# Optimization experiments

Hardware: AMD Instinct MI355X
Metric: run time of the kernel (lower is better)

Reference implementation:

```python
import jax, jax.numpy as jnp
import numpy as np

# dims
N = 2048      # total nodes (64 graphs x 32 nodes)
G = 64        # n_graphs
D = 512       # hidden_dim
H = 8         # n_heads
HD = D // H   # head_dim
E = 16        # edge_features
M = 16384     # n_edges


def setup_inputs() -> dict:
    key = jax.random.key(0)
    ks = jax.random.split(key, 12)
    s = 0.02  # param init scale
    inp = {
        "nodes": jax.random.normal(ks[0], (N, D), jnp.float32),
        "edges": jax.random.normal(ks[1], (M, E), jnp.float32),
        "Wq": jax.random.normal(ks[2], (D, D), jnp.float32) * s,
        "bq": jnp.zeros((D,), jnp.float32),
        "Wk": jax.random.normal(ks[3], (D, D), jnp.float32) * s,
        "bk": jnp.zeros((D,), jnp.float32),
        "Wv": jax.random.normal(ks[4], (D, D), jnp.float32) * s,
        "bv": jnp.zeros((D,), jnp.float32),
        "Wo": jax.random.normal(ks[5], (D, D), jnp.float32) * s,
        "bo": jnp.zeros((D,), jnp.float32),
        "We": jax.random.normal(ks[6], (E, H), jnp.float32) * s,
        "be": jnp.zeros((H,), jnp.float32),
        # 64 graphs of exactly 32 nodes each (sums to N, as jraph requires)
        "n_node": jnp.full((G,), N // G, dtype=jnp.int32),
        "senders": jax.random.randint(ks[7], (M,), 0, N, dtype=jnp.int32),
        "receivers": jax.random.randint(ks[8], (M,), 0, N, dtype=jnp.int32),
    }
    return inp


def reference(nodes, edges, Wq, bq, Wk, bk, Wv, bv, Wo, bo, We, be,
              n_node, senders, receivers):
    scale = HD ** -0.5
    # projections -> [N, H, HD]
    q = (nodes @ Wq + bq).reshape(N, H, HD)
    k = (nodes @ Wk + bk).reshape(N, H, HD)
    v = (nodes @ Wv + bv).reshape(N, H, HD)

    # dense scores [N, N, H]
    attn_scores = jnp.einsum('ihd,jhd->ijh', q, k) * scale

    # block-diagonal graph mask
    graph_indices = jnp.repeat(jnp.arange(G), n_node, total_repeat_length=N)
    same_graph = graph_indices[:, None] == graph_indices[None, :]
    attn_scores = attn_scores + jnp.where(same_graph[:, :, None], 0.0, -1e9)

    # edge bias: project edge features to per-head bias, scatter into [N, N, H]
    edge_bias = edges @ We + be                              # [M, H]
    edge_bias_matrix = jnp.zeros((N, N, H), attn_scores.dtype)
    edge_bias_matrix = edge_bias_matrix.at[receivers, senders].set(edge_bias)
    attn_scores = attn_scores + edge_bias_matrix

    # softmax over keys (axis=1, matching the original)
    attn_weights = jax.nn.softmax(attn_scores, axis=1)

    out = jnp.einsum('ijh,jhd->ihd', attn_weights, v).reshape(N, D)
    return out @ Wo + bo
```

## Files before the change

### kernel.cpp

```cpp
#include <hip/hip_runtime.h>

constexpr int N_NODES = 2048;
constexpr int G       = 64;
constexpr int D       = 512;
constexpr int H       = 8;
constexpr int HD      = 64;
constexpr int E       = 16;
constexpr int M_EDGES = 16384;

typedef __attribute__((ext_vector_type(8))) _Float16 f16x8;
typedef __attribute__((ext_vector_type(4))) float f32x4;

__device__ __forceinline__ void load_lds16(const void* g, void* l) {
    __builtin_amdgcn_global_load_lds(
        (const __attribute__((address_space(1))) unsigned int*)g,
        (__attribute__((address_space(3))) unsigned int*)l, 16, 0, 0);
}

__global__ __launch_bounds__(256) void prep_kernel(
    const float* __restrict__ nodes,
    const float* __restrict__ Wq, const float* __restrict__ Wk,
    const float* __restrict__ Wv, const float* __restrict__ Wo,
    _Float16* __restrict__ nA16, _Float16* __restrict__ wT16)
{
    const int bid = blockIdx.x;
    const int t   = threadIdx.x;

    if (bid < 512) {
        int i = bid * 256 + t;
        float4 v0 = ((const float4*)nodes)[2 * i];
        float4 v1 = ((const float4*)nodes)[2 * i + 1];
        float f[8] = { v0.x, v0.y, v0.z, v0.w, v1.x, v1.y, v1.z, v1.w };
        union { _Float16 h[8]; int4 v; } p;
#pragma unroll
        for (int e = 0; e < 8; ++e) p.h[e] = (_Float16)f[e];
        ((int4*)nA16)[i] = p.v;
        return;
    }

    {
        int idx = bid - 512;
        int z   = idx >> 8;
        int rem = idx & 255;
        int k0  = (rem >> 4) * 32, n0 = (rem & 15) * 32;
        const float* W = (z == 0) ? Wq : (z == 1) ? Wk : (z == 2) ? Wv : Wo;
        __shared__ float tile[32][33];
        {
            int kr = t >> 3, nc4 = (t & 7) * 4;
            float4 v = *(const float4*)(W + (size_t)(k0 + kr) * D + n0 + nc4);
            tile[nc4 + 0][kr] = v.x;
            tile[nc4 + 1][kr] = v.y;
            tile[nc4 + 2][kr] = v.z;
            tile[nc4 + 3][kr] = v.w;
        }
        __syncthreads();
        {
            int nl = t >> 3, kq = (t & 7) * 4;
            union { _Float16 h[4]; uint2 v; } hi;
#pragma unroll
            for (int j = 0; j < 4; ++j)
                hi.h[j] = (_Float16)tile[nl][kq + j];
            size_t base = (size_t)z * D * D + (size_t)(n0 + nl) * D + k0 + kq;
            *(uint2*)(wT16 + base) = hi.v;
        }
    }
}

template <typename CT>
__device__ __forceinline__ void gemm_body(
    const _Float16* __restrict__ A, const _Float16* __restrict__ B,
    const float* __restrict__ bias, CT* __restrict__ C,
    int row0, int col0)
{
    __shared__ __align__(16) char lds[2][2][8192];

    const int t    = threadIdx.x;
    const int lane = t & 63;
    const int w    = t >> 6;
    const int wm   = w >> 1, wn = w & 1;

    const int prow0 = t >> 3;
    const int lslot = (t & 7) ^ (prow0 & 7);

    auto stage = [&](int buf, int k0) {
        size_t a0 = (size_t)(row0 + prow0) * 1024 + k0 * 2 + lslot * 16;
        size_t a1 = a0 + 32 * 1024;
        size_t b0 = (size_t)(col0 + prow0) * 1024 + k0 * 2 + lslot * 16;
        size_t b1 = b0 + 32 * 1024;
        load_lds16((const char*)A + a0, &lds[buf][0][t * 16]);
        load_lds16((const char*)A + a1, &lds[buf][0][4096 + t * 16]);
        load_lds16((const char*)B + b0, &lds[buf][1][t * 16]);
        load_lds16((const char*)B + b1, &lds[buf][1][4096 + t * 16]);
    };

    f32x4 acc[2][2] = {};

    stage(0, 0);
    __syncthreads();

    int cur = 0;
    for (int step = 0; step < 8; ++step) {
        if (step < 7) stage(cur ^ 1, (step + 1) * 64);

        f16x8 fa[2][2], fb[2][2];
#pragma unroll
        for (int mf = 0; mf < 2; ++mf) {
            int row = wm * 32 + mf * 16 + (lane & 15);
#pragma unroll
            for (int ks = 0; ks < 2; ++ks) {
                int ps = ((ks * 4 + (lane >> 4)) ^ (row & 7)) << 4;
                fa[mf][ks] = *(const f16x8*)&lds[cur][0][row * 128 + ps];
            }
        }
#pragma unroll
        for (int nf = 0; nf < 2; ++nf) {
            int row = wn * 32 + nf * 16 + (lane & 15);
#pragma unroll
            for (int ks = 0; ks < 2; ++ks) {
                int ps = ((ks * 4 + (lane >> 4)) ^ (row & 7)) << 4;
                fb[nf][ks] = *(const f16x8*)&lds[cur][1][row * 128 + ps];
            }
        }
#pragma unroll
        for (int mf = 0; mf < 2; ++mf)
#pragma unroll
            for (int nf = 0; nf < 2; ++nf)
#pragma unroll
                for (int ks = 0; ks < 2; ++ks)
                    acc[mf][nf] = __builtin_amdgcn_mfma_f32_16x16x32_f16(
                        fa[mf][ks], fb[nf][ks], acc[mf][nf], 0, 0, 0);

        __syncthreads();
        cur ^= 1;
    }

#pragma unroll
    for (int mf = 0; mf < 2; ++mf)
#pragma unroll
        for (int nf = 0; nf < 2; ++nf) {
            int col = col0 + wn * 32 + nf * 16 + (lane & 15);
            float bv = bias[col];
#pragma unroll
            for (int r = 0; r < 4; ++r) {
                int row = row0 + wm * 32 + mf * 16 + (lane >> 4) * 4 + r;
                C[(size_t)row * D + col] = (CT)(acc[mf][nf][r] + bv);
            }
        }
}

struct GemmArgs {
    const _Float16 *A, *BT;
    const float* bias[3];
    void* C;
};

__global__ __launch_bounds__(256) void gemm_qkv_kernel(GemmArgs a)
{
    const int z = blockIdx.z;
    gemm_body<_Float16>(a.A, a.BT + (size_t)z * D * D, a.bias[z],
                        (_Float16*)a.C + (size_t)z * (size_t)N_NODES * D,
                        blockIdx.y * 64, blockIdx.x * 64);
}

__global__ __launch_bounds__(256) void gemm_out_kernel(GemmArgs a)
{
    gemm_body<float>(a.A, a.BT, a.bias[0], (float*)a.C,
                     blockIdx.y * 64, blockIdx.x * 64);
}

__global__ __launch_bounds__(1024) void attn_kernel(
    const _Float16* __restrict__ QKV16,
    const float* __restrict__ edges, const float* __restrict__ We,
    const float* __restrict__ be,
    const int* __restrict__ snd, const int* __restrict__ rcv,
    _Float16* __restrict__ AO16)
{
    const int g = blockIdx.x;
    const int h = blockIdx.y;
    __shared__ float Qs[32][64];
    __shared__ float Ks[32][65];
    __shared__ float Vs[32][65];
    __shared__ float P[32][33];
    __shared__ int   win[1024];
    __shared__ float WesH[E];

    const int t = threadIdx.x;
    win[t] = -1;
    if (t < E) WesH[t] = We[t * H + h];

    const _Float16* Q16 = QKV16;
    const _Float16* K16 = QKV16 + (size_t)N_NODES * D;
    const _Float16* V16 = QKV16 + (size_t)2 * N_NODES * D;
    for (int idx = t; idx < 32 * 64; idx += 1024) {
        int n = idx >> 6, d = idx & 63;
        size_t ga = (size_t)(g * 32 + n) * D + h * HD + d;
        Qs[n][d] = (float)Q16[ga];
        Ks[n][d] = (float)K16[ga];
        Vs[n][d] = (float)V16[ga];
    }
    __syncthreads();

    for (int it = 0; it < M_EDGES / 1024; ++it) {
        int m = it * 1024 + t;
        int s = snd[m], r = rcv[m];
        if ((s >> 5) == g && (r >> 5) == g)
            atomicMax(&win[((r & 31) << 5) | (s & 31)], m);
    }
    __syncthreads();

    const int i = t >> 5;
    const int j = t & 31;
    float s = 0.f;
#pragma unroll
    for (int d = 0; d < 64; ++d) s += Qs[i][d] * Ks[j][d];
    s *= 0.125f;

    int m = win[(i << 5) | j];
    if (m >= 0) {
        float v = be[h];
#pragma unroll
        for (int e = 0; e < E; ++e) v += edges[m * E + e] * WesH[e];
        s += v;
    }

    float mx = s;
#pragma unroll
    for (int o = 16; o > 0; o >>= 1) mx = fmaxf(mx, __shfl_xor(mx, o));
    float p = __expf(s - mx);
    float sum = p;
#pragma unroll
    for (int o = 16; o > 0; o >>= 1) sum += __shfl_xor(sum, o);
    p /= sum;
    P[i][j] = p;
    __syncthreads();

    float o0 = 0.f, o1 = 0.f;
#pragma unroll
    for (int kk = 0; kk < 32; ++kk) {
        float pv = P[i][kk];
        o0 += pv * Vs[kk][j];
        o1 += pv * Vs[kk][j + 32];
    }
    size_t oa = (size_t)(g * 32 + i) * D + h * HD;
    AO16[oa + j]      = (_Float16)o0;
    AO16[oa + j + 32] = (_Float16)o1;
}

extern "C" void kernel_launch(void* const* d_in, const int* in_sizes, int n_in,
                              void* d_out, int out_size, void* d_ws, size_t ws_size,
                              hipStream_t stream)
{
    const float* nodes = (const float*)d_in[0];
    const float* edges = (const float*)d_in[1];
    const float* Wq    = (const float*)d_in[2];
    const float* bq    = (const float*)d_in[3];
    const float* Wk    = (const float*)d_in[4];
    const float* bk    = (const float*)d_in[5];
    const float* Wv    = (const float*)d_in[6];
    const float* bv    = (const float*)d_in[7];
    const float* Wo    = (const float*)d_in[8];
    const float* bo    = (const float*)d_in[9];
    const float* We    = (const float*)d_in[10];
    const float* be    = (const float*)d_in[11];
    const int* senders   = (const int*)d_in[13];
    const int* receivers = (const int*)d_in[14];

    char* ws = (char*)d_ws;
    _Float16* nA16  = (_Float16*)ws;
    _Float16* wT16  = nA16 + (size_t)N_NODES * D;
    _Float16* QKV16 = wT16 + (size_t)4 * D * D;
    _Float16* AO16  = QKV16 + (size_t)3 * N_NODES * D;

    prep_kernel<<<1536, 256, 0, stream>>>(nodes, Wq, Wk, Wv, Wo, nA16, wT16);

    GemmArgs qkv;
    qkv.A = nA16;
    qkv.BT = wT16;
    qkv.bias[0] = bq; qkv.bias[1] = bk; qkv.bias[2] = bv;
    qkv.C = QKV16;
    gemm_qkv_kernel<<<dim3(D / 64, N_NODES / 64, 3), 256, 0, stream>>>(qkv);

    attn_kernel<<<dim3(G, H), 1024, 0, stream>>>(
        QKV16, edges, We, be, senders, receivers, AO16);

    GemmArgs og;
    og.A = AO16;
    og.BT = wT16 + (size_t)3 * D * D;
    og.bias[0] = bo; og.bias[1] = bo; og.bias[2] = bo;
    og.C = d_out;
    gemm_out_kernel<<<dim3(D / 64, N_NODES / 64), 256, 0, stream>>>(og);
}
```

Measured before the change: 38.20 us.

## Build edge-winner table once globally and shrink attention blocks to 256 threads

Before, each of the 512 attention blocks scanned all 16384 edges to build its own winner table in LDS. Now the table is initialised in the prep kernel and filled once by extra blocks in the QKV GEMM launch, using global atomics. The attention kernel then reads the table, uses 256 threads with 4 scores and 8 outputs per thread, and vectorises the loads and stores. The cost is a global-memory winner buffer and atomics, plus more serial work per thread.

Measured after the change: 33.28 us, median of 2. -12.9%, faster.

```diff
diff --git a/kernel.cpp b/kernel.cpp
--- a/kernel.cpp
+++ b/kernel.cpp
@@ -21,7 +21,8 @@
     const float* __restrict__ nodes,
     const float* __restrict__ Wq, const float* __restrict__ Wk,
     const float* __restrict__ Wv, const float* __restrict__ Wo,
-    _Float16* __restrict__ nA16, _Float16* __restrict__ wT16)
+    _Float16* __restrict__ nA16, _Float16* __restrict__ wT16,
+    int* __restrict__ winner)
 {
     const int bid = blockIdx.x;
     const int t   = threadIdx.x;
@@ -38,7 +39,7 @@
         return;
     }
 
-    {
+    if (bid < 1536) {
         int idx = bid - 512;
         int z   = idx >> 8;
         int rem = idx & 255;
@@ -63,7 +64,10 @@
             size_t base = (size_t)z * D * D + (size_t)(n0 + nl) * D + k0 + kq;
             *(uint2*)(wT16 + base) = hi.v;
         }
-    }
+        return;
+    }
+
+    ((int4*)winner)[(bid - 1536) * 256 + t] = make_int4(-1, -1, -1, -1);
 }
 
 template <typename CT>
@@ -154,9 +158,20 @@
     void* C;
 };
 
-__global__ __launch_bounds__(256) void gemm_qkv_kernel(GemmArgs a)
+__global__ __launch_bounds__(256) void gemm_qkv_kernel(
+    GemmArgs a, const int* __restrict__ snd, const int* __restrict__ rcv,
+    int* __restrict__ winner)
 {
     const int z = blockIdx.z;
+    if (z == 3) {
+        if (blockIdx.y < 8) {
+            int m = (blockIdx.y * 8 + blockIdx.x) * 256 + threadIdx.x;
+            int s = snd[m], r = rcv[m];
+            if ((s >> 5) == (r >> 5))
+                atomicMax(&winner[((r >> 5) << 10) | ((r & 31) << 5) | (s & 31)], m);
+        }
+        return;
+    }
     gemm_body<_Float16>(a.A, a.BT + (size_t)z * D * D, a.bias[z],
                         (_Float16*)a.C + (size_t)z * (size_t)N_NODES * D,
                         blockIdx.y * 64, blockIdx.x * 64);
@@ -168,82 +183,98 @@
                      blockIdx.y * 64, blockIdx.x * 64);
 }
 
-__global__ __launch_bounds__(1024) void attn_kernel(
+__global__ __launch_bounds__(256) void attn_kernel(
     const _Float16* __restrict__ QKV16,
     const float* __restrict__ edges, const float* __restrict__ We,
-    const float* __restrict__ be,
-    const int* __restrict__ snd, const int* __restrict__ rcv,
+    const float* __restrict__ be, const int* __restrict__ winner,
     _Float16* __restrict__ AO16)
 {
     const int g = blockIdx.x;
     const int h = blockIdx.y;
+    const int t = threadIdx.x;
+
     __shared__ float Qs[32][64];
-    __shared__ float Ks[32][65];
-    __shared__ float Vs[32][65];
+    __shared__ float Ks[32][68];
+    __shared__ float Vs[32][68];
     __shared__ float P[32][33];
-    __shared__ int   win[1024];
     __shared__ float WesH[E];
 
-    const int t = threadIdx.x;
-    win[t] = -1;
     if (t < E) WesH[t] = We[t * H + h];
 
-    const _Float16* Q16 = QKV16;
-    const _Float16* K16 = QKV16 + (size_t)N_NODES * D;
-    const _Float16* V16 = QKV16 + (size_t)2 * N_NODES * D;
-    for (int idx = t; idx < 32 * 64; idx += 1024) {
-        int n = idx >> 6, d = idx & 63;
-        size_t ga = (size_t)(g * 32 + n) * D + h * HD + d;
-        Qs[n][d] = (float)Q16[ga];
-        Ks[n][d] = (float)K16[ga];
-        Vs[n][d] = (float)V16[ga];
+    {
+        const int row = t >> 3, c = t & 7;
+        const size_t ga = (size_t)(32 * g + row) * D + h * HD + c * 8;
+#pragma unroll
+        for (int z = 0; z < 3; ++z) {
+            f16x8 v = *(const f16x8*)(QKV16 + (size_t)z * N_NODES * D + ga);
+            float* dst = (z == 0) ? &Qs[row][c * 8]
+                       : (z == 1) ? &Ks[row][c * 8]
+                                  : &Vs[row][c * 8];
+            float4 lo, hi;
+            lo.x = (float)v[0]; lo.y = (float)v[1];
+            lo.z = (float)v[2]; lo.w = (float)v[3];
+            hi.x = (float)v[4]; hi.y = (float)v[5];
+            hi.z = (float)v[6]; hi.w = (float)v[7];
+            *(float4*)(dst)     = lo;
+            *(float4*)(dst + 4) = hi;
+        }
     }
     __syncthreads();
 
-    for (int it = 0; it < M_EDGES / 1024; ++it) {
-        int m = it * 1024 + t;
-        int s = snd[m], r = rcv[m];
-        if ((s >> 5) == g && (r >> 5) == g)
-            atomicMax(&win[((r & 31) << 5) | (s & 31)], m);
+    const int i  = t >> 3;
+    const int j4 = (t & 7) * 4;
+    {
+        float s[4] = {};
+        for (int d = 0; d < HD; ++d) {
+            float qv = Qs[i][d];
+#pragma unroll
+            for (int r = 0; r < 4; ++r)
+                s[r] += qv * Ks[j4 + r][d];
+        }
+        const int* winG = winner + (g << 10);
+        float besH = be[h];
+#pragma unroll
+        for (int r = 0; r < 4; ++r) {
+            s[r] *= 0.125f;
+            int m = winG[(i << 5) | (j4 + r)];
+            if (m >= 0) {
+                float v = besH;
+#pragma unroll
+                for (int e = 0; e < E; ++e) v += edges[m * E + e] * WesH[e];
+                s[r] += v;
+            }
+        }
+        float mx = fmaxf(fmaxf(s[0], s[1]), fmaxf(s[2], s[3]));
+#pragma unroll
+        for (int o = 4; o > 0; o >>= 1) mx = fmaxf(mx, __shfl_xor(mx, o));
+        float p[4], sum = 0.f;
+#pragma unroll
+        for (int r = 0; r < 4; ++r) { p[r] = __expf(s[r] - mx); sum += p[r]; }
+#pragma unroll
+        for (int o = 4; o > 0; o >>= 1) sum += __shfl_xor(sum, o);
+        float inv = 1.0f / sum;
+#pragma unroll
+        for (int r = 0; r < 4; ++r) P[i][j4 + r] = p[r] * inv;
     }
     __syncthreads();
 
-    const int i = t >> 5;
-    const int j = t & 31;
-    float s = 0.f;
-#pragma unroll
-    for (int d = 0; d < 64; ++d) s += Qs[i][d] * Ks[j][d];
-    s *= 0.125f;
-
-    int m = win[(i << 5) | j];
-    if (m >= 0) {
-        float v = be[h];
-#pragma unroll
-        for (int e = 0; e < E; ++e) v += edges[m * E + e] * WesH[e];
-        s += v;
-    }
-
-    float mx = s;
-#pragma unroll
-    for (int o = 16; o > 0; o >>= 1) mx = fmaxf(mx, __shfl_xor(mx, o));
-    float p = __expf(s - mx);
-    float sum = p;
-#pragma unroll
-    for (int o = 16; o > 0; o >>= 1) sum += __shfl_xor(sum, o);
-    p /= sum;
-    P[i][j] = p;
-    __syncthreads();
-
-    float o0 = 0.f, o1 = 0.f;
-#pragma unroll
-    for (int kk = 0; kk < 32; ++kk) {
-        float pv = P[i][kk];
-        o0 += pv * Vs[kk][j];
-        o1 += pv * Vs[kk][j + 32];
-    }
-    size_t oa = (size_t)(g * 32 + i) * D + h * HD;
-    AO16[oa + j]      = (_Float16)o0;
-    AO16[oa + j + 32] = (_Float16)o1;
+    {
+        const int dq = (t & 7) * 8;
+        float o[8] = {};
+        for (int kk = 0; kk < 32; ++kk) {
+            float pv = P[i][kk];
+            float4 v0 = *(const float4*)&Vs[kk][dq];
+            float4 v1 = *(const float4*)&Vs[kk][dq + 4];
+            o[0] += pv * v0.x; o[1] += pv * v0.y;
+            o[2] += pv * v0.z; o[3] += pv * v0.w;
+            o[4] += pv * v1.x; o[5] += pv * v1.y;
+            o[6] += pv * v1.z; o[7] += pv * v1.w;
+        }
+        union { _Float16 h8[8]; int4 v; } pk;
+#pragma unroll
+        for (int dd = 0; dd < 8; ++dd) pk.h8[dd] = (_Float16)o[dd];
+        *(int4*)(AO16 + (size_t)(32 * g + i) * D + h * HD + dq) = pk.v;
+    }
 }
 
 extern "C" void kernel_launch(void* const* d_in, const int* in_sizes, int n_in,
@@ -266,22 +297,25 @@
     const int* receivers = (const int*)d_in[14];
 
     char* ws = (char*)d_ws;
-    _Float16* nA16  = (_Float16*)ws;
-    _Float16* wT16  = nA16 + (size_t)N_NODES * D;
-    _Float16* QKV16 = wT16 + (size_t)4 * D * D;
-    _Float16* AO16  = QKV16 + (size_t)3 * N_NODES * D;
-
-    prep_kernel<<<1536, 256, 0, stream>>>(nodes, Wq, Wk, Wv, Wo, nA16, wT16);
+    _Float16* nA16   = (_Float16*)ws;
+    _Float16* wT16   = nA16 + (size_t)N_NODES * D;
+    _Float16* QKV16  = wT16 + (size_t)4 * D * D;
+    _Float16* AO16   = QKV16 + (size_t)3 * N_NODES * D;
+    int*      winner = (int*)(AO16 + (size_t)N_NODES * D);
+
+    prep_kernel<<<1600, 256, 0, stream>>>(nodes, Wq, Wk, Wv, Wo,
+                                          nA16, wT16, winner);
 
     GemmArgs qkv;
     qkv.A = nA16;
     qkv.BT = wT16;
     qkv.bias[0] = bq; qkv.bias[1] = bk; qkv.bias[2] = bv;
     qkv.C = QKV16;
-    gemm_qkv_kernel<<<dim3(D / 64, N_NODES / 64, 3), 256, 0, stream>>>(qkv);
-
-    attn_kernel<<<dim3(G, H), 1024, 0, stream>>>(
-        QKV16, edges, We, be, senders, receivers, AO16);
+    gemm_qkv_kernel<<<dim3(D / 64, N_NODES / 64, 4), 256, 0, stream>>>(
+        qkv, senders, receivers, winner);
+
+    attn_kernel<<<dim3(G, H), 256, 0, stream>>>(
+        QKV16, edges, We, be, winner, AO16);
 
     GemmArgs og;
     og.A = AO16;
```

## Fuse fp32-to-fp16 conversion and weight transpose into GEMM tile loading

Applied to the files above, without the earlier changes.

Removes the separate prep kernel that converted nodes to fp16 and transposed and converted the weights. The QKV and output GEMMs now read fp32 inputs directly, convert them in registers and write swizzled fp16 tiles to LDS, with register prefetch of the next tile overlapping the MFMA work. The attention kernel's Q/K/V load is also vectorised. This saves one launch and the round trip through the workspace, but weights are reconverted by every block and the LDS stores for B are narrow 4-byte writes.

After: 38.48 us. Within noise of the previous version (+0.7%).

```diff
diff --git a/kernel.cpp b/kernel.cpp
--- a/kernel.cpp
+++ b/kernel.cpp
@@ -17,90 +17,88 @@
         (__attribute__((address_space(3))) unsigned int*)l, 16, 0, 0);
 }
 
-__global__ __launch_bounds__(256) void prep_kernel(
+__global__ __launch_bounds__(256) void gemm_qkv_f32(
     const float* __restrict__ nodes,
     const float* __restrict__ Wq, const float* __restrict__ Wk,
-    const float* __restrict__ Wv, const float* __restrict__ Wo,
-    _Float16* __restrict__ nA16, _Float16* __restrict__ wT16)
+    const float* __restrict__ Wv,
+    const float* __restrict__ bq, const float* __restrict__ bk,
+    const float* __restrict__ bv,
+    _Float16* __restrict__ QKV16)
 {
-    const int bid = blockIdx.x;
-    const int t   = threadIdx.x;
-
-    if (bid < 512) {
-        int i = bid * 256 + t;
-        float4 v0 = ((const float4*)nodes)[2 * i];
-        float4 v1 = ((const float4*)nodes)[2 * i + 1];
-        float f[8] = { v0.x, v0.y, v0.z, v0.w, v1.x, v1.y, v1.z, v1.w };
-        union { _Float16 h[8]; int4 v; } p;
-#pragma unroll
-        for (int e = 0; e < 8; ++e) p.h[e] = (_Float16)f[e];
-        ((int4*)nA16)[i] = p.v;
-        return;
-    }
-
-    {
-        int idx = bid - 512;
-        int z   = idx >> 8;
-        int rem = idx & 255;
-        int k0  = (rem >> 4) * 32, n0 = (rem & 15) * 32;
-        const float* W = (z == 0) ? Wq : (z == 1) ? Wk : (z == 2) ? Wv : Wo;
-        __shared__ float tile[32][33];
-        {
-            int kr = t >> 3, nc4 = (t & 7) * 4;
-            float4 v = *(const float4*)(W + (size_t)(k0 + kr) * D + n0 + nc4);
-            tile[nc4 + 0][kr] = v.x;
-            tile[nc4 + 1][kr] = v.y;
-            tile[nc4 + 2][kr] = v.z;
-            tile[nc4 + 3][kr] = v.w;
-        }
-        __syncthreads();
-        {
-            int nl = t >> 3, kq = (t & 7) * 4;
-            union { _Float16 h[4]; uint2 v; } hi;
-#pragma unroll
-            for (int j = 0; j < 4; ++j)
-                hi.h[j] = (_Float16)tile[nl][kq + j];
-            size_t base = (size_t)z * D * D + (size_t)(n0 + nl) * D + k0 + kq;
-            *(uint2*)(wT16 + base) = hi.v;
-        }
-    }
-}
-
-template <typename CT>
-__device__ __forceinline__ void gemm_body(
-    const _Float16* __restrict__ A, const _Float16* __restrict__ B,
-    const float* __restrict__ bias, CT* __restrict__ C,
-    int row0, int col0)
-{
-    __shared__ __align__(16) char lds[2][2][8192];
+    const int z = blockIdx.z;
+    const float* W    = (z == 0) ? Wq : (z == 1) ? Wk : Wv;
+    const float* bias = (z == 0) ? bq : (z == 1) ? bk : bv;
+    _Float16* C = QKV16 + (size_t)z * (size_t)N_NODES * D;
+
+    const int row0 = blockIdx.y * 64;
+    const int col0 = blockIdx.x * 64;
+
+    __shared__ __align__(16) char As[2][8192];
+    __shared__ __align__(16) char Bs[2][8192];
 
     const int t    = threadIdx.x;
     const int lane = t & 63;
     const int w    = t >> 6;
     const int wm   = w >> 1, wn = w & 1;
 
-    const int prow0 = t >> 3;
-    const int lslot = (t & 7) ^ (prow0 & 7);
-
-    auto stage = [&](int buf, int k0) {
-        size_t a0 = (size_t)(row0 + prow0) * 1024 + k0 * 2 + lslot * 16;
-        size_t a1 = a0 + 32 * 1024;
-        size_t b0 = (size_t)(col0 + prow0) * 1024 + k0 * 2 + lslot * 16;
-        size_t b1 = b0 + 32 * 1024;
-        load_lds16((const char*)A + a0, &lds[buf][0][t * 16]);
-        load_lds16((const char*)A + a1, &lds[buf][0][4096 + t * 16]);
-        load_lds16((const char*)B + b0, &lds[buf][1][t * 16]);
-        load_lds16((const char*)B + b1, &lds[buf][1][4096 + t * 16]);
+    const int ma  = t >> 3;
+    const int sla = t & 7;
+    const int ng  = t & 15;
+    const int kp0 = t >> 4;
+
+    float4 ar[2][2], br[2][2];
+
+    auto issueA = [&](int k0) {
+        const float* p0 = nodes + (size_t)(row0 + ma) * D + k0 + sla * 8;
+        const float* p1 = nodes + (size_t)(row0 + ma + 32) * D + k0 + sla * 8;
+        ar[0][0] = *(const float4*)p0; ar[0][1] = *(const float4*)(p0 + 4);
+        ar[1][0] = *(const float4*)p1; ar[1][1] = *(const float4*)(p1 + 4);
+    };
+    auto issueB = [&](int k0) {
+        const float* q0 = W + (size_t)(k0 + 2 * kp0) * D + col0 + ng * 4;
+        const float* q1 = W + (size_t)(k0 + 2 * (kp0 + 16)) * D + col0 + ng * 4;
+        br[0][0] = *(const float4*)q0; br[0][1] = *(const float4*)(q0 + D);
+        br[1][0] = *(const float4*)q1; br[1][1] = *(const float4*)(q1 + D);
+    };
+    auto writeAB = [&](int buf) {
+#pragma unroll
+        for (int task = 0; task < 2; ++task) {
+            int m = ma + task * 32;
+            float f[8] = { ar[task][0].x, ar[task][0].y, ar[task][0].z, ar[task][0].w,
+                           ar[task][1].x, ar[task][1].y, ar[task][1].z, ar[task][1].w };
+            union { _Float16 h[8]; int4 v; } pk;
+#pragma unroll
+            for (int e = 0; e < 8; ++e) pk.h[e] = (_Float16)f[e];
+            *(int4*)(&As[buf][0] + m * 128 + ((sla ^ (m & 7)) << 4)) = pk.v;
+        }
+#pragma unroll
+        for (int task = 0; task < 2; ++task) {
+            int kk   = 2 * (kp0 + task * 16);
+            int slot = kk >> 3;
+            int off  = (kk & 7) * 2;
+            float l4[4] = { br[task][0].x, br[task][0].y, br[task][0].z, br[task][0].w };
+            float h4[4] = { br[task][1].x, br[task][1].y, br[task][1].z, br[task][1].w };
+#pragma unroll
+            for (int j = 0; j < 4; ++j) {
+                int n = ng * 4 + j;
+                union { _Float16 h[2]; unsigned u; } pk;
+                pk.h[0] = (_Float16)l4[j];
+                pk.h[1] = (_Float16)h4[j];
+                *(unsigned*)(&Bs[buf][0] + n * 128 +
+                             ((slot ^ ((n >> 1) & 7)) << 4) + off) = pk.u;
+            }
+        }
     };
 
     f32x4 acc[2][2] = {};
 
-    stage(0, 0);
+    issueA(0); issueB(0);
+    writeAB(0);
     __syncthreads();
 
     int cur = 0;
     for (int step = 0; step < 8; ++step) {
-        if (step < 7) stage(cur ^ 1, (step + 1) * 64);
+        if (step < 7) { issueA((step + 1) * 64); issueB((step + 1) * 64); }
 
         f16x8 fa[2][2], fb[2][2];
 #pragma unroll
@@ -109,7 +107,7 @@
 #pragma unroll
             for (int ks = 0; ks < 2; ++ks) {
                 int ps = ((ks * 4 + (lane >> 4)) ^ (row & 7)) << 4;
-                fa[mf][ks] = *(const f16x8*)&lds[cur][0][row * 128 + ps];
+                fa[mf][ks] = *(const f16x8*)(&As[cur][0] + row * 128 + ps);
             }
         }
 #pragma unroll
@@ -117,8 +115,8 @@
             int row = wn * 32 + nf * 16 + (lane & 15);
 #pragma unroll
             for (int ks = 0; ks < 2; ++ks) {
-                int ps = ((ks * 4 + (lane >> 4)) ^ (row & 7)) << 4;
-                fb[nf][ks] = *(const f16x8*)&lds[cur][1][row * 128 + ps];
+                int ps = ((ks * 4 + (lane >> 4)) ^ ((row >> 1) & 7)) << 4;
+                fb[nf][ks] = *(const f16x8*)(&Bs[cur][0] + row * 128 + ps);
             }
         }
 #pragma unroll
@@ -130,6 +128,7 @@
                     acc[mf][nf] = __builtin_amdgcn_mfma_f32_16x16x32_f16(
                         fa[mf][ks], fb[nf][ks], acc[mf][nf], 0, 0, 0);
 
+        if (step < 7) writeAB(cur ^ 1);
         __syncthreads();
         cur ^= 1;
     }
@@ -143,29 +142,120 @@
 #pragma unroll
             for (int r = 0; r < 4; ++r) {
                 int row = row0 + wm * 32 + mf * 16 + (lane >> 4) * 4 + r;
-                C[(size_t)row * D + col] = (CT)(acc[mf][nf][r] + bv);
-            }
-        }
-}
-
-struct GemmArgs {
-    const _Float16 *A, *BT;
-    const float* bias[3];
-    void* C;
-};
-
-__global__ __launch_bounds__(256) void gemm_qkv_kernel(GemmArgs a)
+                C[(size_t)row * D + col] = (_Float16)(acc[mf][nf][r] + bv);
+            }
+        }
+}
+
+__global__ __launch_bounds__(256) void gemm_out_f32(
+    const _Float16* __restrict__ AO16, const float* __restrict__ Wo,
+    const float* __restrict__ bo, float* __restrict__ out)
 {
-    const int z = blockIdx.z;
-    gemm_body<_Float16>(a.A, a.BT + (size_t)z * D * D, a.bias[z],
-                        (_Float16*)a.C + (size_t)z * (size_t)N_NODES * D,
-                        blockIdx.y * 64, blockIdx.x * 64);
-}
-
-__global__ __launch_bounds__(256) void gemm_out_kernel(GemmArgs a)
-{
-    gemm_body<float>(a.A, a.BT, a.bias[0], (float*)a.C,
-                     blockIdx.y * 64, blockIdx.x * 64);
+    const int row0 = blockIdx.y * 64;
+    const int col0 = blockIdx.x * 64;
+
+    __shared__ __align__(16) char As[2][8192];
+    __shared__ __align__(16) char Bs[2][8192];
+
+    const int t    = threadIdx.x;
+    const int lane = t & 63;
+    const int w    = t >> 6;
+    const int wm   = w >> 1, wn = w & 1;
+
+    const int prow0 = t >> 3;
+    const int lslot = (t & 7) ^ (prow0 & 7);
+    const int ng  = t & 15;
+    const int kp0 = t >> 4;
+
+    float4 br[2][2];
+
+    auto stageA = [&](int buf, int k0) {
+        size_t a0 = (size_t)(row0 + prow0) * 1024 + k0 * 2 + lslot * 16;
+        size_t a1 = a0 + 32 * 1024;
+        load_lds16((const char*)AO16 + a0, &As[buf][t * 16]);
+        load_lds16((const char*)AO16 + a1, &As[buf][4096 + t * 16]);
+    };
+    auto issueB = [&](int k0) {
+        const float* q0 = Wo + (size_t)(k0 + 2 * kp0) * D + col0 + ng * 4;
+        const float* q1 = Wo + (size_t)(k0 + 2 * (kp0 + 16)) * D + col0 + ng * 4;
+        br[0][0] = *(const float4*)q0; br[0][1] = *(const float4*)(q0 + D);
+        br[1][0] = *(const float4*)q1; br[1][1] = *(const float4*)(q1 + D);
+    };
+    auto writeB = [&](int buf) {
+#pragma unroll
+        for (int task = 0; task < 2; ++task) {
+            int kk   = 2 * (kp0 + task * 16);
+            int slot = kk >> 3;
+            int off  = (kk & 7) * 2;
+            float l4[4] = { br[task][0].x, br[task][0].y, br[task][0].z, br[task][0].w };
+            float h4[4] = { br[task][1].x, br[task][1].y, br[task][1].z, br[task][1].w };
+#pragma unroll
+            for (int j = 0; j < 4; ++j) {
+                int n = ng * 4 + j;
+                union { _Float16 h[2]; unsigned u; } pk;
+                pk.h[0] = (_Float16)l4[j];
+                pk.h[1] = (_Float16)h4[j];
+                *(unsigned*)(&Bs[buf][0] + n * 128 +
+                             ((slot ^ ((n >> 1) & 7)) << 4) + off) = pk.u;
+            }
+        }
+    };
+
+    f32x4 acc[2][2] = {};
+
+    stageA(0, 0); issueB(0);
+    writeB(0);
+    __syncthreads();
+
+    int cur = 0;
+    for (int step = 0; step < 8; ++step) {
+        if (step < 7) { stageA(cur ^ 1, (step + 1) * 64); issueB((step + 1) * 64); }
+
+        f16x8 fa[2][2], fb[2][2];
+#pragma unroll
+        for (int mf = 0; mf < 2; ++mf) {
+            int row = wm * 32 + mf * 16 + (lane & 15);
+#pragma unroll
+            for (int ks = 0; ks < 2; ++ks) {
+                int ps = ((ks * 4 + (lane >> 4)) ^ (row & 7)) << 4;
+                fa[mf][ks] = *(const f16x8*)(&As[cur][0] + row * 128 + ps);
+            }
+        }
+#pragma unroll
+        for (int nf = 0; nf < 2; ++nf) {
+            int row = wn * 32 + nf * 16 + (lane & 15);
+#pragma unroll
+            for (int ks = 0; ks < 2; ++ks) {
+                int ps = ((ks * 4 + (lane >> 4)) ^ ((row >> 1) & 7)) << 4;
+                fb[nf][ks] = *(const f16x8*)(&Bs[cur][0] + row * 128 + ps);
+            }
+        }
+#pragma unroll
+        for (int mf = 0; mf < 2; ++mf)
+#pragma unroll
+            for (int nf = 0; nf < 2; ++nf)
+#pragma unroll
+                for (int ks = 0; ks < 2; ++ks)
+                    acc[mf][nf] = __builtin_amdgcn_mfma_f32_16x16x32_f16(
+                        fa[mf][ks], fb[nf][ks], acc[mf][nf], 0, 0, 0);
+
+        if (step < 7) writeB(cur ^ 1);
+        __syncthreads();
+        cur ^= 1;
+    }
+
+#pragma unroll
+    for (int mf = 0; mf < 2; ++mf)
+#pragma unroll
+        for (int nf = 0; nf < 2; ++nf) {
+            int col = col0 + wn * 32 + nf * 16 + (lane & 15);
+            float bv = bo[col];
+#pragma unroll
+            for (int r = 0; r < 4; ++r) {
+                int row = row0 + wm * 32 + mf * 16 + (lane >> 4) * 4 + r;
+                out[(size_t)row * D + col] = acc[mf][nf][r] + bv;
+            }
+        }
 }
 
 __global__ __launch_bounds__(1024) void attn_kernel(
@@ -177,26 +267,32 @@
 {
     const int g = blockIdx.x;
     const int h = blockIdx.y;
+    const int t = threadIdx.x;
+
     __shared__ float Qs[32][64];
-    __shared__ float Ks[32][65];
-    __shared__ float Vs[32][65];
+    __shared__ float Ks[32][68];
+    __shared__ float Vs[32][68];
     __shared__ float P[32][33];
     __shared__ int   win[1024];
     __shared__ float WesH[E];
 
-    const int t = threadIdx.x;
-    win[t] = -1;
+    win[t & 1023] = -1;
     if (t < E) WesH[t] = We[t * H + h];
 
-    const _Float16* Q16 = QKV16;
-    const _Float16* K16 = QKV16 + (size_t)N_NODES * D;
-    const _Float16* V16 = QKV16 + (size_t)2 * N_NODES * D;
-    for (int idx = t; idx < 32 * 64; idx += 1024) {
-        int n = idx >> 6, d = idx & 63;
-        size_t ga = (size_t)(g * 32 + n) * D + h * HD + d;
-        Qs[n][d] = (float)Q16[ga];
-        Ks[n][d] = (float)K16[ga];
-        Vs[n][d] = (float)V16[ga];
+    if (t < 768) {
+        const int z   = t >> 8;
+        const int v   = t & 255;
+        const int row = v >> 3, c = v & 7;
+        f16x8 x = *(const f16x8*)(QKV16 + (size_t)z * N_NODES * D +
+                                  (size_t)(32 * g + row) * D + h * HD + c * 8);
+        float* dst = (z == 0) ? &Qs[row][c * 8]
+                   : (z == 1) ? &Ks[row][c * 8]
+                              : &Vs[row][c * 8];
+        float4 lo, hi;
+        lo.x = (float)x[0]; lo.y = (float)x[1]; lo.z = (float)x[2]; lo.w = (float)x[3];
+        hi.x = (float)x[4]; hi.y = (float)x[5]; hi.z = (float)x[6]; hi.w = (float)x[7];
+        *(float4*)(dst)     = lo;
+        *(float4*)(dst + 4) = hi;
     }
     __syncthreads();
 
@@ -266,27 +362,15 @@
     const int* receivers = (const int*)d_in[14];
 
     char* ws = (char*)d_ws;
-    _Float16* nA16  = (_Float16*)ws;
-    _Float16* wT16  = nA16 + (size_t)N_NODES * D;
-    _Float16* QKV16 = wT16 + (size_t)4 * D * D;
+    _Float16* QKV16 = (_Float16*)ws;
     _Float16* AO16  = QKV16 + (size_t)3 * N_NODES * D;
 
-    prep_kernel<<<1536, 256, 0, stream>>>(nodes, Wq, Wk, Wv, Wo, nA16, wT16);
-
-    GemmArgs qkv;
-    qkv.A = nA16;
-    qkv.BT = wT16;
-    qkv.bias[0] = bq; qkv.bias[1] = bk; qkv.bias[2] = bv;
-    qkv.C = QKV16;
-    gemm_qkv_kernel<<<dim3(D / 64, N_NODES / 64, 3), 256, 0, stream>>>(qkv);
+    gemm_qkv_f32<<<dim3(D / 64, N_NODES / 64, 3), 256, 0, stream>>>(
+        nodes, Wq, Wk, Wv, bq, bk, bv, QKV16);
 
     attn_kernel<<<dim3(G, H), 1024, 0, stream>>>(
         QKV16, edges, We, be, senders, receivers, AO16);
 
-    GemmArgs og;
-    og.A = AO16;
-    og.BT = wT16 + (size_t)3 * D * D;
-    og.bias[0] = bo; og.bias[1] = bo; og.bias[2] = bo;
-    og.C = d_out;
-    gemm_out_kernel<<<dim3(D / 64, N_NODES / 64), 256, 0, stream>>>(og);
-}
+    gemm_out_f32<<<dim3(D / 64, N_NODES / 64), 256, 0, stream>>>(
+        AO16, Wo, bo, (float*)d_out);
+}
```
